# Kernel optimization log

Hardware: AMD Instinct MI355X
Metric: run time of the kernel (lower is better)

Reference implementation:

```python
import jax, jax.numpy as jnp
import numpy as np

TOP_P = 0.9  # forward default arg, fixed to exercise the top-p path


def setup_inputs() -> dict:
    key = jax.random.key(0)
    k1, k2 = jax.random.split(key)
    B, V = 128, 128000
    logits = jax.random.normal(k1, (B, V), dtype=jnp.float32) * 2.0
    # temperatures in [0.5, 1.5) to avoid divide-by-near-zero
    temperatures = jax.random.uniform(k2, (B,), dtype=jnp.float32, minval=0.5, maxval=1.5)
    return {"logits": logits, "temperatures": temperatures, "top_k": 50}


def reference(logits, temperatures, top_k):
    B, V = logits.shape
    neg_inf = jnp.float32(-jnp.inf)

    # temperature scale + softmax
    scaled = logits.astype(jnp.float32) / temperatures[:, None]
    probs = jax.nn.softmax(scaled, axis=-1)  # (B, V)

    brow = jnp.arange(B)[:, None]

    # top-k filter: keep top-k probs, fill rest with -inf (matches torch scatter into full(-inf))
    if top_k > 0:
        k = min(top_k, V)
        vals, idx = jax.lax.top_k(probs, k)  # (B, k)
        probs = jnp.full_like(probs, neg_inf).at[brow, idx].set(vals)

    # top-p (nucleus) filter: sort desc, cumsum, mask tail beyond top_p (always keep first)
    if TOP_P < 1.0:
        order = jnp.argsort(-probs, axis=-1)              # descending order indices (-inf sorts last)
        sorted_probs = jnp.take_along_axis(probs, order, axis=-1)
        cum = jnp.cumsum(sorted_probs, axis=-1)
        remove = cum > TOP_P
        remove = remove.at[:, 0].set(False)
        sorted_probs = jnp.where(remove, neg_inf, sorted_probs)
        probs = probs.at[brow, order].set(sorted_probs)   # scatter back to original positions

    # Gumbel-max-style sampling: argmax(probs / Exp(1) noise), noise clamped to >= 1e-10
    kn = jax.random.fold_in(jax.random.key(0), 1)
    noise = jnp.maximum(jax.random.exponential(kn, probs.shape, dtype=jnp.float32), 1e-10)
    return jnp.argmax(probs / noise, axis=-1)  # (B,) int tokens
```

## Files before the change

### kernel.cpp

```cpp
#include <hip/hip_runtime.h>
#include <stdint.h>
#include <limits.h>

#define THREEFRY_PARTITIONABLE 1

#define NTK   1024
#define NWAVE (NTK/64)
#define NTK1  512
#define NW1   (NTK1/64)
#define NBUCK 4096
#define CAP   2048
#define CAPS  256
#define CAPG  2048
#define CAPF  512
#define KMAX  512
#define SMAX  32
#define CHUNK_TARGET 16384

#if __has_builtin(__builtin_amdgcn_exp2f)
#define FAST_EXP2(x) __builtin_amdgcn_exp2f(x)
#else
#define FAST_EXP2(x) exp2f(x)
#endif

__device__ __forceinline__ uint32_t rotl32(uint32_t v, int r) {
  return (v << r) | (v >> (32 - r));
}
__device__ __forceinline__ void tfround(uint32_t& x0, uint32_t& x1, int r) {
  x0 += x1; x1 = rotl32(x1, r); x1 ^= x0;
}
__device__ __forceinline__ void threefry2x32(uint32_t k0, uint32_t k1,
                                             uint32_t x0, uint32_t x1,
                                             uint32_t& o0, uint32_t& o1) {
  uint32_t k2 = k0 ^ k1 ^ 0x1BD11BDAu;
  x0 += k0; x1 += k1;
  tfround(x0,x1,13); tfround(x0,x1,15); tfround(x0,x1,26); tfround(x0,x1,6);
  x0 += k1; x1 += k2 + 1u;
  tfround(x0,x1,17); tfround(x0,x1,29); tfround(x0,x1,16); tfround(x0,x1,24);
  x0 += k2; x1 += k0 + 2u;
  tfround(x0,x1,13); tfround(x0,x1,15); tfround(x0,x1,26); tfround(x0,x1,6);
  x0 += k0; x1 += k1 + 3u;
  tfround(x0,x1,17); tfround(x0,x1,29); tfround(x0,x1,16); tfround(x0,x1,24);
  x0 += k1; x1 += k2 + 4u;
  tfround(x0,x1,13); tfround(x0,x1,15); tfround(x0,x1,26); tfround(x0,x1,6);
  x0 += k2; x1 += k0 + 5u;
  o0 = x0; o1 = x1;
}
__device__ __forceinline__ float jax_noise(uint32_t kn0, uint32_t kn1,
                                           unsigned long long i,
                                           unsigned long long total) {
  uint32_t o0, o1, bits;
#if THREEFRY_PARTITIONABLE
  threefry2x32(kn0, kn1, (uint32_t)(i >> 32), (uint32_t)(i & 0xFFFFFFFFull), o0, o1);
  bits = o0 ^ o1;
#else
  unsigned long long H = total >> 1;
  if (i < H) { threefry2x32(kn0, kn1, (uint32_t)i, (uint32_t)(i + H), o0, o1); bits = o0; }
  else       { threefry2x32(kn0, kn1, (uint32_t)(i - H), (uint32_t)i, o0, o1); bits = o1; }
#endif
  float u = __uint_as_float((bits >> 9) | 0x3f800000u) - 1.0f;
  float e = -log1pf(-u);
  return fmaxf(e, 1e-10f);
}
__device__ __forceinline__ uint32_t fkey(float f) {
  uint32_t u = __float_as_uint(f);
  return u ^ ((u >> 31) ? 0xFFFFFFFFu : 0x80000000u);
}
__device__ __forceinline__ float unfkey_floor(uint32_t keyT) {
  if (keyT == 0u) return -INFINITY;
  return __uint_as_float((keyT & 0x80000000u) ? (keyT ^ 0x80000000u) : ~keyT);
}
__device__ __forceinline__ int clamp_k(int k) {
  if (k < 1) k = 1;
  if (k > KMAX) k = KMAX;
  return k;
}

template<int NT, int NW>
__device__ __forceinline__ void block_kth_bucket(uint32_t* hist, uint32_t* wtot,
                                                 int* beta_sh, int k,
                                                 int tid, int lane, int wave) {
  constexpr int BPTc = NBUCK / NT;
  const int base = tid * BPTc;
  uint32_t tsum = 0;
#pragma unroll
  for (int j = 0; j < BPTc; j++) tsum += hist[base + j];
  uint32_t incl = tsum;
  for (int off = 1; off < 64; off <<= 1) {
    uint32_t v = __shfl_down(incl, off);
    if (lane + off < 64) incl += v;
  }
  if (lane == 0) wtot[wave] = incl;
  __syncthreads();
  uint32_t above = incl - tsum;
  for (int w = wave + 1; w < NW; w++) above += wtot[w];
  if (above < (uint32_t)k && above + tsum >= (uint32_t)k) {
    uint32_t run = above;
    for (int j = BPTc - 1; j >= 0; j--) {
      run += hist[base + j];
      if (run >= (uint32_t)k) { *beta_sh = base + j; break; }
    }
  }
  __syncthreads();
}

__global__ __launch_bounds__(NTK1)
void sampler_stream(const float* __restrict__ logits,
                    const float* __restrict__ temps,
                    const int* __restrict__ topk_ptr,
                    float* __restrict__ msArr,
                    double* __restrict__ dsumArr,
                    int* __restrict__ cntArr,
                    float2* __restrict__ pairs,
                    int B, int V, int S, int chunk) {
  const int blk = blockIdx.x;
  const int b = blk / S, sp = blk - b * S;
  const int tid = threadIdx.x, lane = tid & 63, wave = tid >> 6;

  __shared__ uint32_t hist[NBUCK];
  __shared__ float wm[NW1];
  __shared__ double wsum[NW1];
  __shared__ uint32_t wtot[NW1];
  __shared__ int beta_sh, cnum_sh;

  if (tid == 0) { beta_sh = 0; cnum_sh = 0; }
  for (int i = tid; i < NBUCK; i += NTK1) hist[i] = 0;

  const float T = temps[b];
  const float cf = (float)(1.4426950408889634 / (double)T);
  const int k = clamp_k(*topk_ptr);

  const int start = sp * chunk;
  const int end = min(start + chunk, V);
  const float* row = logits + (size_t)b * (size_t)V;
  const int n = (end > start) ? (end - start) : 0;
  const int n4 = n >> 2;
  const float4* row4 = (const float4*)(row + start);

  float v0 = -INFINITY, v1 = -INFINITY, v2 = -INFINITY;
  int   i0 = 0, i1 = 0;
  float a0 = 0.f, a1 = 0.f, a2 = 0.f, a3 = 0.f;

  auto proc = [&](float f, int idx) {
    bool gt0 = f > v0;
    bool gt1 = f > v1;
    bool gt2 = f > v2;
    float nv2 = gt1 ? v1 : (gt2 ? f : v2);
    float nv1 = gt0 ? v0 : (gt1 ? f : v1);
    int   ni1 = gt0 ? i0 : (gt1 ? idx : i1);
    v2 = nv2;
    v1 = nv1; i1 = ni1;
    v0 = gt0 ? f : v0;
    i0 = gt0 ? idx : i0;
  };
  auto proc4 = [&](float4 f, int vb, float& a) {
    proc(f.x, vb); proc(f.y, vb + 1); proc(f.z, vb + 2); proc(f.w, vb + 3);
    a += (FAST_EXP2(f.x * cf) + FAST_EXP2(f.y * cf))
       + (FAST_EXP2(f.z * cf) + FAST_EXP2(f.w * cf));
  };

  int i = tid;
  for (; i + 3 * NTK1 < n4; i += 4 * NTK1) {
    float4 fa = row4[i];
    float4 fb = row4[i + NTK1];
    float4 fc = row4[i + 2 * NTK1];
    float4 fd = row4[i + 3 * NTK1];
    proc4(fa, start + i * 4, a0);
    proc4(fb, start + (i + NTK1) * 4, a1);
    proc4(fc, start + (i + 2 * NTK1) * 4, a2);
    proc4(fd, start + (i + 3 * NTK1) * 4, a3);
  }
  for (; i < n4; i += NTK1) {
    float4 fa = row4[i];
    proc4(fa, start + i * 4, a0);
  }
  for (int v = start + n4 * 4 + tid; v < end; v += NTK1) {
    float f = row[v];
    proc(f, v);
    a0 += FAST_EXP2(f * cf);
  }

  float bm = v0;
  for (int off = 32; off; off >>= 1)
    bm = fmaxf(bm, __shfl_down(bm, off));
  if (lane == 0) wm[wave] = bm;

  double ds = ((double)a0 + (double)a1) + ((double)a2 + (double)a3);
  for (int off = 32; off; off >>= 1)
    ds += __shfl_down(ds, off);
  if (lane == 0) wsum[wave] = ds;
  __syncthreads();

  if (v0 != -INFINITY) atomicAdd(&hist[fkey(v0) >> 20], 1u);
  if (v1 != -INFINITY) atomicAdd(&hist[fkey(v1) >> 20], 1u);
  __syncthreads();

  if (tid == 0) {
    float m_sp = wm[0];
#pragma unroll
    for (int w = 1; w < NW1; w++) m_sp = fmaxf(m_sp, wm[w]);
    msArr[blk] = m_sp;
    double t = 0.0;
    for (int w = 0; w < NW1; w++) t += wsum[w];
    dsumArr[blk] = t;
  }

  block_kth_bucket<NTK1, NW1>(hist, wtot, &beta_sh, k, tid, lane, wave);

  const float fT = unfkey_floor((uint32_t)beta_sh << 20);
  float2* myp = pairs + (size_t)blk * CAPS;

  if (v2 >= fT) {
    for (int i2 = tid; i2 < n4; i2 += NTK1) {
      float4 f = row4[i2];
      const int vb = start + i2 * 4;
      if (f.x >= fT) { int p = atomicAdd(&cnum_sh, 1); if (p < CAPS) myp[p] = make_float2(f.x, __int_as_float(vb)); }
      if (f.y >= fT) { int p = atomicAdd(&cnum_sh, 1); if (p < CAPS) myp[p] = make_float2(f.y, __int_as_float(vb + 1)); }
      if (f.z >= fT) { int p = atomicAdd(&cnum_sh, 1); if (p < CAPS) myp[p] = make_float2(f.z, __int_as_float(vb + 2)); }
      if (f.w >= fT) { int p = atomicAdd(&cnum_sh, 1); if (p < CAPS) myp[p] = make_float2(f.w, __int_as_float(vb + 3)); }
    }
    for (int v = start + n4 * 4 + tid; v < end; v += NTK1) {
      float f = row[v];
      if (f >= fT) { int p = atomicAdd(&cnum_sh, 1); if (p < CAPS) myp[p] = make_float2(f, __int_as_float(v)); }
    }
  } else {
    if (v0 >= fT) { int p = atomicAdd(&cnum_sh, 1); if (p < CAPS) myp[p] = make_float2(v0, __int_as_float(i0)); }
    if (v1 >= fT) { int p = atomicAdd(&cnum_sh, 1); if (p < CAPS) myp[p] = make_float2(v1, __int_as_float(i1)); }
  }
  __syncthreads();
  if (tid == 0) cntArr[blk] = min(cnum_sh, CAPS);
}

__global__ __launch_bounds__(NTK, 1)
void sampler_finalize(const float* __restrict__ temps,
                      const int* __restrict__ topk_ptr,
                      const float* __restrict__ msArr,
                      const double* __restrict__ dsumArr,
                      const int* __restrict__ cntArr,
                      const float2* __restrict__ pairs,
                      int* __restrict__ out,
                      int B, int V, int S) {
  const int b = blockIdx.x;
  const int tid = threadIdx.x, lane = tid & 63, wave = tid >> 6;

  __shared__ uint32_t hist[NBUCK];
  __shared__ float cv[CAPG];
  __shared__ int   ci[CAPG];
  __shared__ float c2v[CAPF];
  __shared__ int   c2i[CAPF];
  __shared__ float c2p[CAPF];
  __shared__ float sv[KMAX];
  __shared__ int   si[KMAX];
  __shared__ float sc[KMAX];
  __shared__ uint32_t wtot[NWAVE];
  __shared__ int   offL[SMAX + 1];
  __shared__ int   cnL[SMAX];
  __shared__ float msL[SMAX];
  __shared__ double dsL[SMAX];
  __shared__ int   beta_sh, cnt2_sh, L_sh;
  __shared__ float m_sh, D_sh;

  const int k = clamp_k(*topk_ptr);
  const float T = temps[b];

  if (tid == 0) { beta_sh = 0; cnt2_sh = 0; }
  if (tid < S) {
    msL[tid] = msArr[b * S + tid];
    dsL[tid] = dsumArr[b * S + tid];
    int c = cntArr[b * S + tid];
    cnL[tid] = (c < CAPS) ? c : CAPS;
  }
  for (int i = tid; i < NBUCK; i += NTK) hist[i] = 0;
  __syncthreads();

  if (tid == 0) {
    int acc = 0;
    for (int j = 0; j < S; j++) { offL[j] = acc; acc += cnL[j]; }
    offL[S] = acc;
    float mg = msL[0];
    for (int j = 1; j < S; j++) mg = fmaxf(mg, msL[j]);
    double t = 0.0;
    for (int j = 0; j < S; j++) t += dsL[j];
    const double cd = 1.4426950408889634 / (double)T;
    D_sh = (float)(t * exp2(-(double)mg * cd));
    m_sh = mg / T;
  }
  __syncthreads();

  const int TC = min(offL[S], CAPG);

  for (int t = tid; t < TC; t += NTK) {
    int j = 0;
#pragma unroll
    for (int jj = 1; jj <= SMAX; jj++)
      if (jj <= S) j += (t >= offL[jj]);
    float2 pr = pairs[(size_t)(b * S + j) * CAPS + (t - offL[j])];
    cv[t] = pr.x;
    ci[t] = __float_as_int(pr.y);
    atomicAdd(&hist[fkey(pr.x) >> 20], 1u);
  }
  __syncthreads();

  block_kth_bucket<NTK, NWAVE>(hist, wtot, &beta_sh, k, tid, lane, wave);

  const float fT = unfkey_floor((uint32_t)beta_sh << 20);
  for (int t = tid; t < TC; t += NTK) {
    float val = cv[t];
    if (val >= fT) {
      int pos = atomicAdd(&cnt2_sh, 1);
      if (pos < CAPF) { c2v[pos] = val; c2i[pos] = ci[t]; }
    }
  }
  __syncthreads();

  const int C = min(cnt2_sh, CAPF);
  const float m = m_sh, D = D_sh;
  for (int t = tid; t < C; t += NTK)
    c2p[t] = expf(c2v[t] / T - m) / D;
  __syncthreads();

  for (int t = tid; t < C; t += NTK) {
    float pi = c2p[t];
    int   ii = c2i[t];
    int r = 0;
    for (int j = 0; j < C; j++) {
      float pj = c2p[j];
      r += (pj > pi) || (pj == pi && c2i[j] < ii);
    }
    if (r < k) { sv[r] = pi; si[r] = ii; }
  }
  __syncthreads();

  const int kk = (k < C) ? k : C;

  {
    uint32_t kn0, kn1;
    threefry2x32(0u, 0u, 0u, 1u, kn0, kn1);
    unsigned long long total = (unsigned long long)B * (unsigned long long)V;
    for (int j = tid; j < kk; j += NTK) {
      unsigned long long flat = (unsigned long long)b * (unsigned long long)V
                              + (unsigned long long)si[j];
      sc[j] = sv[j] / jax_noise(kn0, kn1, flat, total);
    }
  }

  if (tid == 0) {
    float cum = 0.f;
    int L = 1;
    bool stop = false;
    for (int j0 = 0; j0 < kk && !stop; j0 += 8) {
      float t0 = sv[j0],     t1 = sv[j0 + 1], t2 = sv[j0 + 2], t3 = sv[j0 + 3];
      float t4 = sv[j0 + 4], t5 = sv[j0 + 5], t6 = sv[j0 + 6], t7 = sv[j0 + 7];
      float tt[8] = {t0, t1, t2, t3, t4, t5, t6, t7};
#pragma unroll
      for (int q = 0; q < 8; q++) {
        int j = j0 + q;
        if (j >= kk) { stop = true; break; }
        cum += tt[q];
        if (j == 0) continue;
        if (cum <= 0.9f) L = j + 1;
        else { stop = true; break; }
      }
    }
    L_sh = L;
  }
  __syncthreads();

  if (wave == 0) {
    const int L = L_sh;
    float bs = -1.0f;
    int   bi = INT_MAX;
    for (int j = lane; j < L; j += 64) {
      float s = sc[j];
      int   ix = si[j];
      if (s > bs || (s == bs && ix < bi)) { bs = s; bi = ix; }
    }
    for (int off = 32; off; off >>= 1) {
      float os = __shfl_down(bs, off);
      int   oi = __shfl_down(bi, off);
      if (os > bs || (os == bs && oi < bi)) { bs = os; bi = oi; }
    }
    if (lane == 0) out[b] = bi;
  }
}

__global__ __launch_bounds__(NTK, 1)
void sampler_fused(const float* __restrict__ logits,
                   const float* __restrict__ temps,
                   const int* __restrict__ topk_ptr,
                   int* __restrict__ out,
                   int B, int V) {
  const int b = blockIdx.x;
  const int tid = threadIdx.x, lane = tid & 63, wave = tid >> 6;

  __shared__ uint32_t hist[NBUCK];
  __shared__ float cv[CAP];
  __shared__ int   ci[CAP];
  __shared__ float cp[CAP];
  __shared__ float sv[KMAX];
  __shared__ int   si[KMAX];
  __shared__ float sc[KMAX];
  __shared__ float wm[NWAVE];
  __shared__ double wsum[NWAVE];
  __shared__ uint32_t wtot[NWAVE];
  __shared__ int beta_sh, cnum_sh, L_sh;
  __shared__ float m_sh, D_sh;

  if (tid == 0) { beta_sh = 0; cnum_sh = 0; }
  for (int i = tid; i < NBUCK; i += NTK) hist[i] = 0;
  __syncthreads();

  const float T = temps[b];
  const float cf = (float)(1.4426950408889634 / (double)T);
  const int k = clamp_k(*topk_ptr);
  const float* row = logits + (size_t)b * (size_t)V;
  const int n4 = ((V & 3) == 0) ? (V >> 2) : 0;
  const float4* row4 = (const float4*)row;

  float v0 = -INFINITY, v1 = -INFINITY, v2 = -INFINITY;
  int   i0 = 0, i1 = 0;
  float a0 = 0.f, a1 = 0.f, a2 = 0.f, a3 = 0.f;

  auto proc = [&](float f, int idx) {
    bool gt0 = f > v0;
    bool gt1 = f > v1;
    bool gt2 = f > v2;
    float nv2 = gt1 ? v1 : (gt2 ? f : v2);
    float nv1 = gt0 ? v0 : (gt1 ? f : v1);
    int   ni1 = gt0 ? i0 : (gt1 ? idx : i1);
    v2 = nv2;
    v1 = nv1; i1 = ni1;
    v0 = gt0 ? f : v0;
    i0 = gt0 ? idx : i0;
  };
  auto proc4 = [&](float4 f, int vb, float& a) {
    proc(f.x, vb); proc(f.y, vb + 1); proc(f.z, vb + 2); proc(f.w, vb + 3);
    a += (FAST_EXP2(f.x * cf) + FAST_EXP2(f.y * cf))
       + (FAST_EXP2(f.z * cf) + FAST_EXP2(f.w * cf));
  };

  int i = tid;
  if (i + 7 * NTK < n4) {
    float4 A0 = row4[i];
    float4 A1 = row4[i + NTK];
    float4 A2 = row4[i + 2 * NTK];
    float4 A3 = row4[i + 3 * NTK];
    float4 A4 = row4[i + 4 * NTK];
    float4 A5 = row4[i + 5 * NTK];
    float4 A6 = row4[i + 6 * NTK];
    float4 A7 = row4[i + 7 * NTK];
    int ia = i;
    i += 8 * NTK;
    while (i + 7 * NTK < n4) {
      float4 B0 = row4[i];
      float4 B1 = row4[i + NTK];
      float4 B2 = row4[i + 2 * NTK];
      float4 B3 = row4[i + 3 * NTK];
      float4 B4 = row4[i + 4 * NTK];
      float4 B5 = row4[i + 5 * NTK];
      float4 B6 = row4[i + 6 * NTK];
      float4 B7 = row4[i + 7 * NTK];
      proc4(A0, ia * 4, a0);
      proc4(A1, (ia + NTK) * 4, a1);
      proc4(A2, (ia + 2 * NTK) * 4, a2);
      proc4(A3, (ia + 3 * NTK) * 4, a3);
      proc4(A4, (ia + 4 * NTK) * 4, a0);
      proc4(A5, (ia + 5 * NTK) * 4, a1);
      proc4(A6, (ia + 6 * NTK) * 4, a2);
      proc4(A7, (ia + 7 * NTK) * 4, a3);
      A0 = B0; A1 = B1; A2 = B2; A3 = B3;
      A4 = B4; A5 = B5; A6 = B6; A7 = B7;
      ia = i;
      i += 8 * NTK;
    }
    proc4(A0, ia * 4, a0);
    proc4(A1, (ia + NTK) * 4, a1);
    proc4(A2, (ia + 2 * NTK) * 4, a2);
    proc4(A3, (ia + 3 * NTK) * 4, a3);
    proc4(A4, (ia + 4 * NTK) * 4, a0);
    proc4(A5, (ia + 5 * NTK) * 4, a1);
    proc4(A6, (ia + 6 * NTK) * 4, a2);
    proc4(A7, (ia + 7 * NTK) * 4, a3);
  }
  for (; i + 3 * NTK < n4; i += 4 * NTK) {
    float4 fa = row4[i];
    float4 fb = row4[i + NTK];
    float4 fc = row4[i + 2 * NTK];
    float4 fd = row4[i + 3 * NTK];
    proc4(fa, i * 4, a0);
    proc4(fb, (i + NTK) * 4, a1);
    proc4(fc, (i + 2 * NTK) * 4, a2);
    proc4(fd, (i + 3 * NTK) * 4, a3);
  }
  for (; i < n4; i += NTK) {
    float4 fa = row4[i];
    proc4(fa, i * 4, a0);
  }
  for (int v = n4 * 4 + tid; v < V; v += NTK) {
    float f = row[v];
    proc(f, v);
    a0 += FAST_EXP2(f * cf);
  }

  float bm = v0;
  for (int off = 32; off; off >>= 1)
    bm = fmaxf(bm, __shfl_down(bm, off));
  if (lane == 0) wm[wave] = bm;

  double ds = ((double)a0 + (double)a1) + ((double)a2 + (double)a3);
  for (int off = 32; off; off >>= 1)
    ds += __shfl_down(ds, off);
  if (lane == 0) wsum[wave] = ds;

  if (v0 != -INFINITY) atomicAdd(&hist[fkey(v0) >> 20], 1u);
  if (v1 != -INFINITY) atomicAdd(&hist[fkey(v1) >> 20], 1u);
  __syncthreads();

  if (tid == 0) {
    float mg = wm[0];
#pragma unroll
    for (int w = 1; w < NWAVE; w++) mg = fmaxf(mg, wm[w]);
    double t = 0.0;
    for (int w = 0; w < NWAVE; w++) t += wsum[w];
    const double cd = 1.4426950408889634 / (double)T;
    D_sh = (float)(t * exp2(-(double)mg * cd));
    m_sh = mg / T;
  }

  block_kth_bucket<NTK, NWAVE>(hist, wtot, &beta_sh, k, tid, lane, wave);

  const float fT = unfkey_floor((uint32_t)beta_sh << 20);
  auto emit1 = [&](float f, int idx) {
    if (f >= fT) {
      int p = atomicAdd(&cnum_sh, 1);
      if (p < CAP) { cv[p] = f; ci[p] = idx; }
    }
  };
  if (v2 >= fT) {
    for (int i2 = tid; i2 < n4; i2 += NTK) {
      float4 f = row4[i2];
      const int vb = i2 * 4;
      emit1(f.x, vb); emit1(f.y, vb + 1); emit1(f.z, vb + 2); emit1(f.w, vb + 3);
    }
    for (int v = n4 * 4 + tid; v < V; v += NTK) emit1(row[v], v);
  } else {
    if (v0 >= fT) { int p = atomicAdd(&cnum_sh, 1); if (p < CAP) { cv[p] = v0; ci[p] = i0; } }
    if (v1 >= fT) { int p = atomicAdd(&cnum_sh, 1); if (p < CAP) { cv[p] = v1; ci[p] = i1; } }
  }
  __syncthreads();

  const int C = min(cnum_sh, CAP);
  const float m = m_sh, D = D_sh;
  for (int t = tid; t < C; t += NTK)
    cp[t] = expf(cv[t] / T - m) / D;
  __syncthreads();

  for (int t = tid; t < C; t += NTK) {
    float pi = cp[t];
    int   ii = ci[t];
    int r = 0;
    for (int j = 0; j < C; j++) {
      float pj = cp[j];
      r += (pj > pi) || (pj == pi && ci[j] < ii);
    }
    if (r < k) { sv[r] = pi; si[r] = ii; }
  }
  __syncthreads();

  const int kk = (k < C) ? k : C;
  {
    uint32_t kn0, kn1;
    threefry2x32(0u, 0u, 0u, 1u, kn0, kn1);
    unsigned long long total = (unsigned long long)B * (unsigned long long)V;
    for (int j = tid; j < kk; j += NTK) {
      unsigned long long flat = (unsigned long long)b * (unsigned long long)V
                              + (unsigned long long)si[j];
      sc[j] = sv[j] / jax_noise(kn0, kn1, flat, total);
    }
  }
  if (tid == 0) {
    float cum = 0.f;
    int L = 1;
    bool stop = false;
    for (int j0 = 0; j0 < kk && !stop; j0 += 8) {
      float t0 = sv[j0],     t1 = sv[j0 + 1], t2 = sv[j0 + 2], t3 = sv[j0 + 3];
      float t4 = sv[j0 + 4], t5 = sv[j0 + 5], t6 = sv[j0 + 6], t7 = sv[j0 + 7];
      float tt[8] = {t0, t1, t2, t3, t4, t5, t6, t7};
#pragma unroll
      for (int q = 0; q < 8; q++) {
        int j = j0 + q;
        if (j >= kk) { stop = true; break; }
        cum += tt[q];
        if (j == 0) continue;
        if (cum <= 0.9f) L = j + 1;
        else { stop = true; break; }
      }
    }
    L_sh = L;
  }
  __syncthreads();

  if (wave == 0) {
    const int L = L_sh;
    float bs = -1.0f;
    int   bi = INT_MAX;
    for (int j = lane; j < L; j += 64) {
      float s = sc[j];
      int   ix = si[j];
      if (s > bs || (s == bs && ix < bi)) { bs = s; bi = ix; }
    }
    for (int off = 32; off; off >>= 1) {
      float os = __shfl_down(bs, off);
      int   oi = __shfl_down(bi, off);
      if (os > bs || (os == bs && oi < bi)) { bs = os; bi = oi; }
    }
    if (lane == 0) out[b] = bi;
  }
}

extern "C" void kernel_launch(void* const* d_in, const int* in_sizes, int n_in,
                              void* d_out, int out_size, void* d_ws, size_t ws_size,
                              hipStream_t stream) {
  const float* logits = (const float*)d_in[0];
  const float* temps  = (const float*)d_in[1];
  const int*   topk   = (const int*)d_in[2];
  int* out = (int*)d_out;

  int B = in_sizes[1];
  int V = in_sizes[0] / B;

  int S = (V + CHUNK_TARGET - 1) / CHUNK_TARGET;
  if (S > SMAX) S = SMAX;
  if (S < 1) S = 1;
  size_t need;
  for (;;) {
    need = (size_t)B * S * (sizeof(double) + sizeof(float) + sizeof(int))
         + (size_t)B * S * CAPS * sizeof(float2);
    if (need <= ws_size || S <= 2) break;
    S >>= 1;
  }

  if (ws_size < need || S < 2) {
    sampler_fused<<<dim3(B), dim3(NTK), 0, stream>>>(logits, temps, topk, out, B, V);
    return;
  }

  int chunk = (((V + S - 1) / S) + 3) & ~3;

  double* dsumArr = (double*)d_ws;
  float*  msArr   = (float*)(dsumArr + (size_t)B * S);
  int*    cntArr  = (int*)(msArr + (size_t)B * S);
  float2* pairs   = (float2*)(cntArr + (size_t)B * S);

  sampler_stream<<<dim3(B * S), dim3(NTK1), 0, stream>>>(
      logits, temps, topk, msArr, dsumArr, cntArr, pairs, B, V, S, chunk);
  sampler_finalize<<<dim3(B), dim3(NTK), 0, stream>>>(
      temps, topk, msArr, dsumArr, cntArr, pairs, out, B, V, S);
}
```

Measured before the change: 116.6 us.

## Fuse stream and finalize kernels via per-row last-block ticket

Merges the per-chunk streaming kernel and the per-row finalize kernel into one launch. Each chunk block increments a per-row atomic counter after writing its partial results, and the last block for a row does the finalize work, reusing the histogram shared memory for the sorted top-k arrays. A small init kernel zeroes the counters. This aims to remove the second kernel launch and its grid-wide dependency gap, at the cost of more shared memory per block (which may reduce occupancy of the streaming phase) and finalize running with 512 rather than 1024 threads.

```diff
diff --git a/kernel.cpp b/kernel.cpp
--- a/kernel.cpp
+++ b/kernel.cpp
@@ -104,24 +104,41 @@
   __syncthreads();
 }
 
+__global__ void sampler_init(int* __restrict__ rowCnt, int B) {
+  int t = blockIdx.x * blockDim.x + threadIdx.x;
+  if (t < B) rowCnt[t] = 0;
+}
+
 __global__ __launch_bounds__(NTK1)
-void sampler_stream(const float* __restrict__ logits,
-                    const float* __restrict__ temps,
-                    const int* __restrict__ topk_ptr,
-                    float* __restrict__ msArr,
-                    double* __restrict__ dsumArr,
-                    int* __restrict__ cntArr,
-                    float2* __restrict__ pairs,
-                    int B, int V, int S, int chunk) {
+void sampler_mega(const float* __restrict__ logits,
+                  const float* __restrict__ temps,
+                  const int* __restrict__ topk_ptr,
+                  float* __restrict__ msArr,
+                  double* __restrict__ dsumArr,
+                  int* __restrict__ cntArr,
+                  float2* __restrict__ pairs,
+                  int* __restrict__ rowCnt,
+                  int* __restrict__ out,
+                  int B, int V, int S, int chunk) {
   const int blk = blockIdx.x;
   const int b = blk / S, sp = blk - b * S;
   const int tid = threadIdx.x, lane = tid & 63, wave = tid >> 6;
 
   __shared__ uint32_t hist[NBUCK];
+  __shared__ float cv[CAPG];
+  __shared__ int   ci[CAPG];
+  __shared__ float c2v[CAPF];
+  __shared__ int   c2i[CAPF];
+  __shared__ float c2p[CAPF];
   __shared__ float wm[NW1];
   __shared__ double wsum[NW1];
   __shared__ uint32_t wtot[NW1];
-  __shared__ int beta_sh, cnum_sh;
+  __shared__ int   offL[SMAX + 1];
+  __shared__ int   cnL[SMAX];
+  __shared__ float msL[SMAX];
+  __shared__ double dsL[SMAX];
+  __shared__ int beta_sh, cnum_sh, L_sh, ticket_sh;
+  __shared__ float m_sh, D_sh;
 
   if (tid == 0) { beta_sh = 0; cnum_sh = 0; }
   for (int i = tid; i < NBUCK; i += NTK1) hist[i] = 0;
@@ -229,48 +246,25 @@
   }
   __syncthreads();
   if (tid == 0) cntArr[blk] = min(cnum_sh, CAPS);
-}
-
-__global__ __launch_bounds__(NTK, 1)
-void sampler_finalize(const float* __restrict__ temps,
-                      const int* __restrict__ topk_ptr,
-                      const float* __restrict__ msArr,
-                      const double* __restrict__ dsumArr,
-                      const int* __restrict__ cntArr,
-                      const float2* __restrict__ pairs,
-                      int* __restrict__ out,
-                      int B, int V, int S) {
-  const int b = blockIdx.x;
-  const int tid = threadIdx.x, lane = tid & 63, wave = tid >> 6;
-
-  __shared__ uint32_t hist[NBUCK];
-  __shared__ float cv[CAPG];
-  __shared__ int   ci[CAPG];
-  __shared__ float c2v[CAPF];
-  __shared__ int   c2i[CAPF];
-  __shared__ float c2p[CAPF];
-  __shared__ float sv[KMAX];
-  __shared__ int   si[KMAX];
-  __shared__ float sc[KMAX];
-  __shared__ uint32_t wtot[NWAVE];
-  __shared__ int   offL[SMAX + 1];
-  __shared__ int   cnL[SMAX];
-  __shared__ float msL[SMAX];
-  __shared__ double dsL[SMAX];
-  __shared__ int   beta_sh, cnt2_sh, L_sh;
-  __shared__ float m_sh, D_sh;
-
-  const int k = clamp_k(*topk_ptr);
-  const float T = temps[b];
-
-  if (tid == 0) { beta_sh = 0; cnt2_sh = 0; }
+
+  __syncthreads();
+  if (tid == 0) {
+    __threadfence();
+    ticket_sh = atomicAdd(&rowCnt[b], 1);
+  }
+  __syncthreads();
+  if (ticket_sh != S - 1) return;
+  if (tid == 0) __threadfence();
+  __syncthreads();
+
+  if (tid == 0) { beta_sh = 0; cnum_sh = 0; }
   if (tid < S) {
     msL[tid] = msArr[b * S + tid];
     dsL[tid] = dsumArr[b * S + tid];
     int c = cntArr[b * S + tid];
     cnL[tid] = (c < CAPS) ? c : CAPS;
   }
-  for (int i = tid; i < NBUCK; i += NTK) hist[i] = 0;
+  for (int t = tid; t < NBUCK; t += NTK1) hist[t] = 0;
   __syncthreads();
 
   if (tid == 0) {
@@ -289,7 +283,7 @@
 
   const int TC = min(offL[S], CAPG);
 
-  for (int t = tid; t < TC; t += NTK) {
+  for (int t = tid; t < TC; t += NTK1) {
     int j = 0;
 #pragma unroll
     for (int jj = 1; jj <= SMAX; jj++)
@@ -301,25 +295,28 @@
   }
   __syncthreads();
 
-  block_kth_bucket<NTK, NWAVE>(hist, wtot, &beta_sh, k, tid, lane, wave);
-
-  const float fT = unfkey_floor((uint32_t)beta_sh << 20);
-  for (int t = tid; t < TC; t += NTK) {
+  block_kth_bucket<NTK1, NW1>(hist, wtot, &beta_sh, k, tid, lane, wave);
+  float* sv = (float*)hist;
+  int*   si = (int*)hist + KMAX;
+  float* sc = (float*)hist + 2 * KMAX;
+
+  const float fT2 = unfkey_floor((uint32_t)beta_sh << 20);
+  for (int t = tid; t < TC; t += NTK1) {
     float val = cv[t];
-    if (val >= fT) {
-      int pos = atomicAdd(&cnt2_sh, 1);
+    if (val >= fT2) {
+      int pos = atomicAdd(&cnum_sh, 1);
       if (pos < CAPF) { c2v[pos] = val; c2i[pos] = ci[t]; }
     }
   }
   __syncthreads();
 
-  const int C = min(cnt2_sh, CAPF);
+  const int C = min(cnum_sh, CAPF);
   const float m = m_sh, D = D_sh;
-  for (int t = tid; t < C; t += NTK)
+  for (int t = tid; t < C; t += NTK1)
     c2p[t] = expf(c2v[t] / T - m) / D;
   __syncthreads();
 
-  for (int t = tid; t < C; t += NTK) {
+  for (int t = tid; t < C; t += NTK1) {
     float pi = c2p[t];
     int   ii = c2i[t];
     int r = 0;
@@ -337,7 +334,7 @@
     uint32_t kn0, kn1;
     threefry2x32(0u, 0u, 0u, 1u, kn0, kn1);
     unsigned long long total = (unsigned long long)B * (unsigned long long)V;
-    for (int j = tid; j < kk; j += NTK) {
+    for (int j = tid; j < kk; j += NTK1) {
       unsigned long long flat = (unsigned long long)b * (unsigned long long)V
                               + (unsigned long long)si[j];
       sc[j] = sv[j] / jax_noise(kn0, kn1, flat, total);
@@ -635,7 +632,8 @@
   size_t need;
   for (;;) {
     need = (size_t)B * S * (sizeof(double) + sizeof(float) + sizeof(int))
-         + (size_t)B * S * CAPS * sizeof(float2);
+         + (size_t)B * S * CAPS * sizeof(float2)
+         + (size_t)B * sizeof(int);
     if (need <= ws_size || S <= 2) break;
     S >>= 1;
   }
@@ -651,9 +649,9 @@
   float*  msArr   = (float*)(dsumArr + (size_t)B * S);
   int*    cntArr  = (int*)(msArr + (size_t)B * S);
   float2* pairs   = (float2*)(cntArr + (size_t)B * S);
-
-  sampler_stream<<<dim3(B * S), dim3(NTK1), 0, stream>>>(
-      logits, temps, topk, msArr, dsumArr, cntArr, pairs, B, V, S, chunk);
-  sampler_finalize<<<dim3(B), dim3(NTK), 0, stream>>>(
-      temps, topk, msArr, dsumArr, cntArr, pairs, out, B, V, S);
-}
+  int*    rowCnt  = (int*)(pairs + (size_t)B * S * CAPS);
+
+  sampler_init<<<dim3((B + 255) / 256), dim3(256), 0, stream>>>(rowCnt, B);
+  sampler_mega<<<dim3(B * S), dim3(NTK1), 0, stream>>>(
+      logits, temps, topk, msArr, dsumArr, cntArr, pairs, rowCnt, out, B, V, S, chunk);
+}
```

Measured after the change: 147.5 us. +26.5%, slower.
